# Performance work log

Hardware: AMD Instinct MI355X
Metric: run time of the kernel (lower is better)

Reference implementation:

```python
import jax, jax.numpy as jnp
import numpy as np

N_NODES = 100000
N_EDGES = 1000000
D = 64  # gat_input_size == gat_hidden_size
NEG_SLOPE = 0.2  # PyG GATConv default leaky_relu slope


def setup_inputs() -> dict:
    key = jax.random.key(0)
    k1, k2, k3, k4, k5, k6 = jax.random.split(key, 6)
    g = jax.random.normal(k1, (N_NODES, D), dtype=jnp.float32)
    edge_index = jax.random.randint(k2, (2, N_EDGES), 0, N_NODES, dtype=jnp.int32)
    scale = 1.0 / np.sqrt(D)
    W = jax.random.normal(k3, (D, D), dtype=jnp.float32) * scale
    att_src = jax.random.normal(k4, (D,), dtype=jnp.float32) * scale
    att_dst = jax.random.normal(k5, (D,), dtype=jnp.float32) * scale
    bias = jnp.zeros((D,), dtype=jnp.float32)
    return {"g": g, "edge_index": edge_index, "W": W,
            "att_src": att_src, "att_dst": att_dst, "bias": bias}


def _gat_layer(x, src, dst, W, att_src, att_dst, bias):
    N = x.shape[0]
    h = x @ W                               # [N, D] projected features
    a_src = h @ att_src                     # [N] per-node source logits
    a_dst = h @ att_dst                     # [N] per-node target logits
    e = jax.nn.leaky_relu(a_src[src] + a_dst[dst], NEG_SLOPE)  # [E]
    # numerically stable segment softmax over edges grouped by target node
    m = jax.ops.segment_max(e, dst, num_segments=N)            # [N]
    m = jnp.where(jnp.isfinite(m), m, 0.0)                     # isolated nodes
    ex = jnp.exp(e - m[dst])                                   # [E]
    denom = jax.ops.segment_sum(ex, dst, num_segments=N)       # [N]
    alpha = ex / (denom[dst] + 1e-16)                          # [E]
    out = jax.ops.segment_sum(alpha[:, None] * h[src], dst, num_segments=N)
    return out + bias


def reference(g, edge_index, W, att_src, att_dst, bias):
    src, dst = edge_index[0], edge_index[1]
    for _ in range(4):  # same shared GAT applied 4 times
        g = _gat_layer(g, src, dst, W, att_src, att_dst, bias)
    return g
```

## Files before the change

### kernel.cpp

```cpp
#include <hip/hip_runtime.h>
#include <hip/hip_bf16.h>

typedef unsigned int u32;
typedef unsigned short u16;
typedef unsigned long long u64;
typedef __attribute__((ext_vector_type(8))) short short8;
typedef __attribute__((ext_vector_type(4))) float f32x4;
typedef __attribute__((ext_vector_type(2))) float f32x2;

#define LRELU_SLOPE 0.2f
#define BPB 32
#define MAXPER 13000

__device__ inline float bfbits(u32 hi) { union { u32 i; float f; } v; v.i = hi; return v.f; }
__device__ inline float bflo(u32 w) { return bfbits(w << 16); }
__device__ inline float bfhi(u32 w) { return bfbits(w & 0xFFFF0000u); }
__device__ inline float bf2f(u16 s) { return bfbits(((u32)s) << 16); }
__device__ inline u16 f2bf(float f) {
  union { float f; u32 i; } v; v.f = f;
  u32 r = v.i + 0x7FFFu + ((v.i >> 16) & 1u);
  return (u16)(r >> 16);
}
__device__ inline f32x2 up2(u32 w) { return (f32x2){bflo(w), bfhi(w)}; }

__device__ inline int xcd_swz(int orig, int nwg) {
  int xcd = orig & 7, idx = orig >> 3;
  int q = nwg >> 3, r = nwg & 7;
  return (xcd < r ? xcd * (q + 1) : r * (q + 1) + (xcd - r) * q) + idx;
}

__global__ void dp_kernel(const u32* __restrict__ g, int nwords, int* __restrict__ mode,
                          const void* __restrict__ W, const void* __restrict__ as,
                          const void* __restrict__ ad, const void* __restrict__ bs,
                          float* __restrict__ pf, u16* __restrict__ wfrag,
                          int* __restrict__ gcnt) {
  __shared__ int cnt;
  if (threadIdx.x == 0) cnt = 0;
  if (threadIdx.x < 8) gcnt[threadIdx.x] = 0;
  __syncthreads();
  int c = 0;
  for (int i = threadIdx.x; i < nwords; i += 256) {
    u32 e = g[i] & 0x7F80u;
    if (e >= 0x3000u && e <= 0x4180u) c++;
  }
  atomicAdd(&cnt, c);
  __syncthreads();
  int md = (2 * cnt > nwords) ? 1 : 0;
  if (threadIdx.x == 0) *mode = md;

  for (int i = threadIdx.x; i < 4288; i += 256) {
    const void* p; int j;
    if (i < 4096)      { p = W;  j = i; }
    else if (i < 4160) { p = as; j = i - 4096; }
    else if (i < 4224) { p = ad; j = i - 4160; }
    else               { p = bs; j = i - 4224; }
    pf[i] = md ? bf2f(((const u16*)p)[j]) : ((const float*)p)[j];
  }
  __syncthreads();
  for (int i = threadIdx.x; i < 4096; i += 256) {
    int f = i >> 9, lane = (i >> 3) & 63, j = i & 7;
    int cc = f >> 1, t = f & 1;
    int k = 32 * t + 8 * (lane >> 4) + j;
    int n = 16 * cc + (lane & 15);
    wfrag[i] = f2bf(pf[k * 64 + n]);
  }
}

__device__ void binA_body(const int* __restrict__ src, const int* __restrict__ dst,
                          int* __restrict__ gcnt, uint2* __restrict__ binned,
                          int E, int nper, int cap, int bid) {
  __shared__ int lcnt[8], lbase[8], lcur[8];
  const int K = 8;
  int tile0 = bid * (256 * K);
  int t = threadIdx.x;
  if (t < 8) { lcnt[t] = 0; lcur[t] = 0; }
  __syncthreads();
  int dv[K], sv[K], bv[K];
#pragma unroll
  for (int j = 0; j < K; ++j) {
    int idx = tile0 + j * 256 + t;
    bool ok = idx < E;
    int d = ok ? __builtin_nontemporal_load(&dst[idx]) : 0;
    int s = ok ? __builtin_nontemporal_load(&src[idx]) : 0;
    int b = -1;
    if (ok) {
      b = (d >= 4 * nper) ? 4 : 0;
      if (d >= (b + 2) * nper) b += 2;
      if (d >= (b + 1) * nper) b += 1;
      atomicAdd(&lcnt[b], 1);
    }
    dv[j] = d; sv[j] = s; bv[j] = b;
  }
  __syncthreads();
  if (t < 8) lbase[t] = atomicAdd(&gcnt[t], lcnt[t]);
  __syncthreads();
#pragma unroll
  for (int j = 0; j < K; ++j) {
    int b = bv[j];
    if (b >= 0) {
      int slot = lbase[b] + atomicAdd(&lcur[b], 1);
      if (slot < cap) binned[(size_t)b * cap + slot] = make_uint2((u32)sv[j], (u32)dv[j]);
    }
  }
}

__device__ void proj0_body(const void* __restrict__ graw, const int* __restrict__ mode,
                           const u16* __restrict__ wfrag, const float* __restrict__ pf,
                           u16* __restrict__ h0, u16* __restrict__ h1,
                           float* __restrict__ as0, float* __restrict__ as1,
                           float* __restrict__ ad0, int N, int bid, int pblocks) {
  if (bid == 0) {
    if (threadIdx.x < 32)       ((u32*)(h0 + (size_t)N * 64))[threadIdx.x] = 0u;
    else if (threadIdx.x < 64)  ((u32*)(h1 + (size_t)N * 64))[threadIdx.x - 32] = 0u;
    else if (threadIdx.x == 64) as0[N] = -1e30f;
    else if (threadIdx.x == 65) as1[N] = -1e30f;
  }
  int lane = threadIdx.x & 63;
  int quad = lane >> 4, m = lane & 15;
  int wtile = (int)(((size_t)bid * 256 + threadIdx.x) >> 6);
  int ntiles = (N + 15) >> 4;
  int nwaves = pblocks * 4;

  int md = *mode;
  bool f32in = (md == 0);

  short8 bfrag[8];
#pragma unroll
  for (int f = 0; f < 8; ++f)
    bfrag[f] = *(const short8*)(wfrag + f * 512 + lane * 8);
  float asv[4], adv[4];
#pragma unroll
  for (int c = 0; c < 4; ++c) {
    asv[c] = pf[4096 + 16 * c + m];
    adv[c] = pf[4160 + 16 * c + m];
  }

  for (int tile = wtile; tile < ntiles; tile += nwaves) {
    int row0 = tile << 4;
    int rl = row0 + m; if (rl > N - 1) rl = N - 1;
    short8 a0, a1;
    if (f32in) {
      const float* xr = (const float*)graw + (size_t)rl * 64 + 8 * quad;
      float4 f0 = *(const float4*)(xr);
      float4 f1 = *(const float4*)(xr + 4);
      float4 f2 = *(const float4*)(xr + 32);
      float4 f3 = *(const float4*)(xr + 36);
      a0[0] = (short)f2bf(f0.x); a0[1] = (short)f2bf(f0.y);
      a0[2] = (short)f2bf(f0.z); a0[3] = (short)f2bf(f0.w);
      a0[4] = (short)f2bf(f1.x); a0[5] = (short)f2bf(f1.y);
      a0[6] = (short)f2bf(f1.z); a0[7] = (short)f2bf(f1.w);
      a1[0] = (short)f2bf(f2.x); a1[1] = (short)f2bf(f2.y);
      a1[2] = (short)f2bf(f2.z); a1[3] = (short)f2bf(f2.w);
      a1[4] = (short)f2bf(f3.x); a1[5] = (short)f2bf(f3.y);
      a1[6] = (short)f2bf(f3.z); a1[7] = (short)f2bf(f3.w);
    } else {
      const u16* xr = (const u16*)graw + (size_t)rl * 64 + 8 * quad;
      a0 = *(const short8*)(xr);
      a1 = *(const short8*)(xr + 32);
    }

    f32x4 acc[4];
#pragma unroll
    for (int c = 0; c < 4; ++c) {
      f32x4 z = {0.f, 0.f, 0.f, 0.f};
      z = __builtin_amdgcn_mfma_f32_16x16x32_bf16(a0, bfrag[2 * c + 0], z, 0, 0, 0);
      z = __builtin_amdgcn_mfma_f32_16x16x32_bf16(a1, bfrag[2 * c + 1], z, 0, 0, 0);
      acc[c] = z;
    }

#pragma unroll
    for (int r = 0; r < 4; ++r) {
      int row = row0 + 4 * quad + r;
      float v0 = acc[0][r], v1 = acc[1][r], v2 = acc[2][r], v3 = acc[3][r];
      if (row < N) {
        u16* hr = h0 + (size_t)row * 64 + m;
        hr[0]  = f2bf(v0);
        hr[16] = f2bf(v1);
        hr[32] = f2bf(v2);
        hr[48] = f2bf(v3);
      }
      float s1 = v0 * asv[0] + v1 * asv[1] + v2 * asv[2] + v3 * asv[3];
      float s2 = v0 * adv[0] + v1 * adv[1] + v2 * adv[2] + v3 * adv[3];
#pragma unroll
      for (int msk = 1; msk <= 8; msk <<= 1) {
        s1 += __shfl_xor(s1, msk, 64);
        s2 += __shfl_xor(s2, msk, 64);
      }
      if (m == 0 && row < N) { as0[row] = s1; ad0[row] = s2; }
    }
  }
}

__global__ void __launch_bounds__(256) fatBP_kernel(
    const int* __restrict__ src, const int* __restrict__ dst, int* __restrict__ gcnt,
    uint2* __restrict__ binned, int E, int nper, int cap, int abl,
    const void* __restrict__ graw, const int* __restrict__ mode,
    const u16* __restrict__ wfrag, const float* __restrict__ pf,
    u16* __restrict__ h0, u16* __restrict__ h1,
    float* __restrict__ as0, float* __restrict__ as1,
    float* __restrict__ ad0, int N) {
  if ((int)blockIdx.x < abl) {
    binA_body(src, dst, gcnt, binned, E, nper, cap, (int)blockIdx.x);
  } else {
    proj0_body(graw, mode, wfrag, pf, h0, h1, as0, as1, ad0, N,
               (int)blockIdx.x - abl, (int)gridDim.x - abl);
  }
}

__global__ void __launch_bounds__(256) binA_kernel(
    const int* __restrict__ src, const int* __restrict__ dst, int* __restrict__ gcnt,
    uint2* __restrict__ binned, int E, int nper, int cap) {
  binA_body(src, dst, gcnt, binned, E, nper, cap, (int)blockIdx.x);
}
__global__ void __launch_bounds__(256) proj0_kernel(
    const void* __restrict__ graw, const int* __restrict__ mode,
    const u16* __restrict__ wfrag, const float* __restrict__ pf,
    u16* __restrict__ h0, u16* __restrict__ h1,
    float* __restrict__ as0, float* __restrict__ as1,
    float* __restrict__ ad0, int N) {
  proj0_body(graw, mode, wfrag, pf, h0, h1, as0, as1, ad0, N,
             (int)blockIdx.x, (int)gridDim.x);
}

__global__ void __launch_bounds__(256) histA_kernel(
    const uint2* __restrict__ binned, const int* __restrict__ gcnt,
    u32* __restrict__ slices, int nper, int cap) {
  __shared__ u32 cnt_lds[MAXPER];
  int b = blockIdx.x & 7;
  int j = blockIdx.x >> 3;
  int cnt = gcnt[b]; if (cnt > cap) cnt = cap;
  int chunk = (cnt + BPB - 1) / BPB;
  int begin = j * chunk;
  int endc = begin + chunk; if (endc > cnt) endc = cnt;
  for (int k = threadIdx.x; k < nper; k += 256) cnt_lds[k] = 0;
  __syncthreads();
  const uint2* reg = binned + (size_t)b * cap;
  int kbase = b * nper;
  for (int i = begin + threadIdx.x; i < endc; i += 256)
    atomicAdd(&cnt_lds[(int)reg[i].y - kbase], 1u);
  __syncthreads();
  u32* out = slices + (size_t)(b * BPB + j) * nper;
  for (int k = threadIdx.x; k < nper; k += 256) out[k] = cnt_lds[k];
}

__global__ void scan1f_kernel(const u32* __restrict__ slices, int* __restrict__ row_off,
                              int* __restrict__ partials, int nper, int N) {
  __shared__ int smem[1024];
  int t = threadIdx.x;
  int idx = blockIdx.x * 1024 + t;
  int v = 0;
  if (idx < N) {
    int b = idx / nper;
    int kk = idx - b * nper;
    const u32* s = slices + (size_t)b * BPB * nper + kk;
    u32 tt = 0;
#pragma unroll 8
    for (int j = 0; j < BPB; ++j) tt += s[(size_t)j * nper];
    v = (int)((tt + 7u) & ~7u);
  }
  smem[t] = v;
  __syncthreads();
  for (int off = 1; off < 1024; off <<= 1) {
    int u = (t >= off) ? smem[t - off] : 0;
    __syncthreads();
    smem[t] += u;
    __syncthreads();
  }
  if (idx < N) row_off[idx + 1] = smem[t];
  if (t == 1023) partials[blockIdx.x] = smem[t];
}

__global__ void scan3c_kernel(int* __restrict__ row_off, const int* __restrict__ partials,
                              int P, u32* __restrict__ slices, int* __restrict__ csr_src,
                              int nper, int N, int dummy) {
  __shared__ int smem[1024];
  int t = threadIdx.x;
  int pv = (t < P) ? partials[t] : 0;
  smem[t] = pv;
  __syncthreads();
  for (int off = 1; off < 1024; off <<= 1) {
    int u = (t >= off) ? smem[t - off] : 0;
    __syncthreads();
    smem[t] += u;
    __syncthreads();
  }
  int blk = blockIdx.x;
  int prefix = (blk > 0) ? smem[blk - 1] : 0;
  int idx = blk * 1024 + t;
  if (idx == 0) row_off[0] = 0;
  if (idx < N) {
    int vend = row_off[idx + 1] + prefix;
    row_off[idx + 1] = vend;
    int b = idx / nper;
    int kk = idx - b * nper;
    u32* s = slices + (size_t)b * BPB * nper + kk;
    u32 tv[BPB];
    u32 deg = 0;
#pragma unroll
    for (int j = 0; j < BPB; ++j) { tv[j] = s[(size_t)j * nper]; deg += tv[j]; }
    u32 pdeg = (deg + 7u) & ~7u;
    u32 run = (u32)vend - pdeg;
#pragma unroll
    for (int j = 0; j < BPB; ++j) { s[(size_t)j * nper] = run; run += tv[j]; }
    for (u32 p = run; p < (u32)vend; ++p) csr_src[p] = dummy;
  }
}

__global__ void __launch_bounds__(256) scatterB_kernel(
    const uint2* __restrict__ binned, const int* __restrict__ gcnt,
    const u32* __restrict__ slices, int* __restrict__ csr_src, int nper, int cap) {
  __shared__ u32 base_lds[MAXPER];
  int b = blockIdx.x & 7;
  int j = blockIdx.x >> 3;
  int cnt = gcnt[b]; if (cnt > cap) cnt = cap;
  int chunk = (cnt + BPB - 1) / BPB;
  int begin = j * chunk;
  int endc = begin + chunk; if (endc > cnt) endc = cnt;
  const u32* s = slices + (size_t)(b * BPB + j) * nper;
  for (int k = threadIdx.x; k < nper; k += 256) base_lds[k] = s[k];
  __syncthreads();
  const uint2* reg = binned + (size_t)b * cap;
  int kbase = b * nper;
  for (int i = begin + threadIdx.x; i < endc; i += 256) {
    uint2 r = reg[i];
    u32 p = atomicAdd(&base_lds[(int)r.y - kbase], 1u);
    csr_src[p] = (int)r.x;
  }
}

__global__ void hist_local_kernel(const uint2* __restrict__ binned, const int* __restrict__ gcnt,
                                  int* __restrict__ deg, int cap) {
  int b = blockIdx.x & 7;
  int vb = blockIdx.x >> 3, nvb = gridDim.x >> 3;
  int cnt = gcnt[b]; if (cnt > cap) cnt = cap;
  const uint2* reg = binned + (size_t)b * cap;
  for (int i = vb * blockDim.x + threadIdx.x; i < cnt; i += nvb * blockDim.x)
    atomicAdd(&deg[reg[i].y], 1);
}

__global__ void scatter_local_kernel(const uint2* __restrict__ binned, const int* __restrict__ gcnt,
                                     int* __restrict__ cursor, int* __restrict__ csr_src, int cap) {
  int b = blockIdx.x & 7;
  int vb = blockIdx.x >> 3, nvb = gridDim.x >> 3;
  int cnt = gcnt[b]; if (cnt > cap) cnt = cap;
  const uint2* reg = binned + (size_t)b * cap;
  for (int i = vb * blockDim.x + threadIdx.x; i < cnt; i += nvb * blockDim.x) {
    uint2 r = reg[i];
    int p = atomicAdd(&cursor[r.y], 1);
    csr_src[p] = (int)r.x;
  }
}

__global__ void scan1_kernel(const int* __restrict__ deg, int* __restrict__ row_off,
                             int* __restrict__ partials, int N) {
  __shared__ int smem[1024];
  int t = threadIdx.x;
  int idx = blockIdx.x * 1024 + t;
  int v = (idx < N) ? (int)(((u32)deg[idx] + 7u) & ~7u) : 0;
  smem[t] = v;
  __syncthreads();
  for (int off = 1; off < 1024; off <<= 1) {
    int u = (t >= off) ? smem[t - off] : 0;
    __syncthreads();
    smem[t] += u;
    __syncthreads();
  }
  if (idx < N) row_off[idx + 1] = smem[t];
  if (t == 1023) partials[blockIdx.x] = smem[t];
}

__global__ void scan2_kernel(int* __restrict__ partials, int P) {
  __shared__ int smem[1024];
  int t = threadIdx.x;
  int v = (t < P) ? partials[t] : 0;
  smem[t] = v;
  __syncthreads();
  for (int off = 1; off < 1024; off <<= 1) {
    int u = (t >= off) ? smem[t - off] : 0;
    __syncthreads();
    smem[t] += u;
    __syncthreads();
  }
  if (t < P) partials[t] = smem[t];
}

__global__ void scan3_kernel(int* __restrict__ row_off, const int* __restrict__ partials,
                             int* __restrict__ cursor, int N) {
  int b = blockIdx.x;
  int idx = b * 1024 + threadIdx.x;
  if (idx < N) {
    int v = row_off[idx + 1] + ((b > 0) ? partials[b - 1] : 0);
    row_off[idx + 1] = v;
    if (idx + 1 < N) cursor[idx + 1] = v;
  }
  if (idx == 0) { row_off[0] = 0; cursor[0] = 0; }
}

__global__ void padC_kernel(const int* __restrict__ row_off, const int* __restrict__ cursor,
                            int* __restrict__ csr_src, int N, int dummy) {
  int i = blockIdx.x * blockDim.x + threadIdx.x;
  if (i >= N) return;
  int e = row_off[i + 1];
  for (int p = cursor[i]; p < e; ++p) csr_src[p] = dummy;
}

__global__ void __launch_bounds__(256) fusedFG_kernel(
    const u16* __restrict__ hin, const float* __restrict__ asi,
    const float* __restrict__ adi, u16* __restrict__ hout,
    float* __restrict__ aso, float* __restrict__ ado,
    const int* __restrict__ row_off, const int* __restrict__ csr_src,
    const float* __restrict__ pf, const u16* __restrict__ wfrag, int N) {
  __shared__ u16 xs[16][72];
  __shared__ float sred[2][16][4];

  int tid = threadIdx.x;
  int lane = tid & 63;
  int w = tid >> 6;
  int quad = lane >> 4, m = lane & 15;
  int grp = lane >> 4;
  int eg = (lane >> 3) & 1;
  int fg = lane & 7;
  int tile = xcd_swz((int)blockIdx.x, (int)gridDim.x);
  int row_in = w * 4 + grp;
  int i = tile * 16 + row_in;
  bool valid = i < N;

  short8 bf0 = *(const short8*)(wfrag + (2 * w + 0) * 512 + lane * 8);
  short8 bf1 = *(const short8*)(wfrag + (2 * w + 1) * 512 + lane * 8);
  float asw = pf[4096 + 16 * w + m];
  float adw = pf[4160 + 16 * w + m];

  int beg = 0, end = 0;
  float advv = 0.f;
  if (valid) { beg = row_off[i]; end = row_off[i + 1]; advv = adi[i]; }

  f32x2 acc0 = {0.f, 0.f}, acc1 = {0.f, 0.f}, acc2 = {0.f, 0.f}, acc3 = {0.f, 0.f};
  float den = 0.f;
  for (int b0 = beg; b0 < end; b0 += 8) {
    int eA = b0 + eg;
    int sA = csr_src[eA];
    int sB = csr_src[eA + 2];
    int sC = csr_src[eA + 4];
    int sD = csr_src[eA + 6];
    float aA = asi[sA];
    float aB = asi[sB];
    float aC = asi[sC];
    float aD = asi[sD];
    uint4 hA = ((const uint4*)(hin + (size_t)sA * 64))[fg];
    uint4 hB = ((const uint4*)(hin + (size_t)sB * 64))[fg];
    uint4 hC = ((const uint4*)(hin + (size_t)sC * 64))[fg];
    uint4 hD = ((const uint4*)(hin + (size_t)sD * 64))[fg];

    float tA = aA + advv; tA = (tA > 0.f) ? tA : LRELU_SLOPE * tA;
    float tB = aB + advv; tB = (tB > 0.f) ? tB : LRELU_SLOPE * tB;
    float tC = aC + advv; tC = (tC > 0.f) ? tC : LRELU_SLOPE * tC;
    float tD = aD + advv; tD = (tD > 0.f) ? tD : LRELU_SLOPE * tD;
    float wA = __expf(fminf(tA, 60.f));
    float wB = __expf(fminf(tB, 60.f));
    float wC = __expf(fminf(tC, 60.f));
    float wD = __expf(fminf(tD, 60.f));
    den += (wA + wB) + (wC + wD);
    f32x2 wA2 = {wA, wA}, wB2 = {wB, wB}, wC2 = {wC, wC}, wD2 = {wD, wD};
    acc0 += wA2 * up2(hA.x); acc0 += wB2 * up2(hB.x);
    acc0 += wC2 * up2(hC.x); acc0 += wD2 * up2(hD.x);
    acc1 += wA2 * up2(hA.y); acc1 += wB2 * up2(hB.y);
    acc1 += wC2 * up2(hC.y); acc1 += wD2 * up2(hD.y);
    acc2 += wA2 * up2(hA.z); acc2 += wB2 * up2(hB.z);
    acc2 += wC2 * up2(hC.z); acc2 += wD2 * up2(hD.z);
    acc3 += wA2 * up2(hA.w); acc3 += wB2 * up2(hB.w);
    acc3 += wC2 * up2(hC.w); acc3 += wD2 * up2(hD.w);
  }
  den += __shfl_xor(den, 8, 64);
#pragma unroll
  for (int c = 0; c < 2; ++c) {
    acc0[c] += __shfl_xor(acc0[c], 8, 64);
    acc1[c] += __shfl_xor(acc1[c], 8, 64);
    acc2[c] += __shfl_xor(acc2[c], 8, 64);
    acc3[c] += __shfl_xor(acc3[c], 8, 64);
  }
  float inv = (den > 0.f) ? 1.f / den : 0.f;
  float oa[8] = {acc0[0], acc0[1], acc1[0], acc1[1],
                 acc2[0], acc2[1], acc3[0], acc3[1]};

  if (!eg) {
    u32 o[4];
    if (valid) {
#pragma unroll
      for (int j = 0; j < 4; ++j) {
        float v0 = oa[2 * j]     * inv + pf[4224 + 8 * fg + 2 * j];
        float v1 = oa[2 * j + 1] * inv + pf[4224 + 8 * fg + 2 * j + 1];
        o[j] = (u32)f2bf(v0) | ((u32)f2bf(v1) << 16);
      }
    } else {
      o[0] = o[1] = o[2] = o[3] = 0u;
    }
    *(uint4*)&xs[row_in][fg * 8] = make_uint4(o[0], o[1], o[2], o[3]);
  }
  __syncthreads();

  short8 a0 = *(const short8*)&xs[m][8 * quad];
  short8 a1 = *(const short8*)&xs[m][32 + 8 * quad];
  f32x4 z = {0.f, 0.f, 0.f, 0.f};
  z = __builtin_amdgcn_mfma_f32_16x16x32_bf16(a0, bf0, z, 0, 0, 0);
  z = __builtin_amdgcn_mfma_f32_16x16x32_bf16(a1, bf1, z, 0, 0, 0);
#pragma unroll
  for (int r = 0; r < 4; ++r) {
    int row = tile * 16 + 4 * quad + r;
    if (row < N) hout[(size_t)row * 64 + 16 * w + m] = f2bf(z[r]);
    float s1 = z[r] * asw, s2 = z[r] * adw;
#pragma unroll
    for (int msk = 1; msk <= 8; msk <<= 1) {
      s1 += __shfl_xor(s1, msk, 64);
      s2 += __shfl_xor(s2, msk, 64);
    }
    if (m == 0) { sred[0][4 * quad + r][w] = s1; sred[1][4 * quad + r][w] = s2; }
  }
  __syncthreads();
  if (tid < 32) {
    int row = tid & 15, sel = tid >> 4;
    float v = sred[sel][row][0] + sred[sel][row][1] + sred[sel][row][2] + sred[sel][row][3];
    int gr = tile * 16 + row;
    if (gr < N) (sel ? ado : aso)[gr] = v;
  }
}

__global__ void __launch_bounds__(256) gatherL_kernel(
    const u16* __restrict__ h, const float* __restrict__ a_src,
    const float* __restrict__ a_dst, const int* __restrict__ row_off,
    const int* __restrict__ csr_src, const float* __restrict__ pf,
    void* __restrict__ dout, int N, const int* __restrict__ mode) {
  int lane = threadIdx.x & 63;
  int grp = lane >> 4;
  int eg  = (lane >> 3) & 1;
  int fg  = lane & 7;
  int w   = threadIdx.x >> 6;
  int tile = xcd_swz((int)blockIdx.x, (int)gridDim.x);
  int i = tile * 16 + w * 4 + grp;
  bool valid = i < N;

  int beg = 0, end = 0;
  float adv = 0.f;
  if (valid) {
    beg = row_off[i];
    end = row_off[i + 1];
    adv = a_dst[i];
  }

  f32x2 acc0 = {0.f, 0.f}, acc1 = {0.f, 0.f}, acc2 = {0.f, 0.f}, acc3 = {0.f, 0.f};
  float den = 0.f;

  for (int b0 = beg; b0 < end; b0 += 8) {
    int eA = b0 + eg;
    int sA = csr_src[eA];
    int sB = csr_src[eA + 2];
    int sC = csr_src[eA + 4];
    int sD = csr_src[eA + 6];
    float aA = a_src[sA];
    float aB = a_src[sB];
    float aC = a_src[sC];
    float aD = a_src[sD];
    uint4 hA = ((const uint4*)(h + (size_t)sA * 64))[fg];
    uint4 hB = ((const uint4*)(h + (size_t)sB * 64))[fg];
    uint4 hC = ((const uint4*)(h + (size_t)sC * 64))[fg];
    uint4 hD = ((const uint4*)(h + (size_t)sD * 64))[fg];

    float tA = aA + adv; tA = (tA > 0.f) ? tA : LRELU_SLOPE * tA;
    float tB = aB + adv; tB = (tB > 0.f) ? tB : LRELU_SLOPE * tB;
    float tC = aC + adv; tC = (tC > 0.f) ? tC : LRELU_SLOPE * tC;
    float tD = aD + adv; tD = (tD > 0.f) ? tD : LRELU_SLOPE * tD;
    float wA = __expf(fminf(tA, 60.f));
    float wB = __expf(fminf(tB, 60.f));
    float wC = __expf(fminf(tC, 60.f));
    float wD = __expf(fminf(tD, 60.f));
    den += (wA + wB) + (wC + wD);
    f32x2 wA2 = {wA, wA}, wB2 = {wB, wB}, wC2 = {wC, wC}, wD2 = {wD, wD};
    acc0 += wA2 * up2(hA.x); acc0 += wB2 * up2(hB.x);
    acc0 += wC2 * up2(hC.x); acc0 += wD2 * up2(hD.x);
    acc1 += wA2 * up2(hA.y); acc1 += wB2 * up2(hB.y);
    acc1 += wC2 * up2(hC.y); acc1 += wD2 * up2(hD.y);
    acc2 += wA2 * up2(hA.z); acc2 += wB2 * up2(hB.z);
    acc2 += wC2 * up2(hC.z); acc2 += wD2 * up2(hD.z);
    acc3 += wA2 * up2(hA.w); acc3 += wB2 * up2(hB.w);
    acc3 += wC2 * up2(hC.w); acc3 += wD2 * up2(hD.w);
  }

  den += __shfl_xor(den, 8, 64);
#pragma unroll
  for (int c = 0; c < 2; ++c) {
    acc0[c] += __shfl_xor(acc0[c], 8, 64);
    acc1[c] += __shfl_xor(acc1[c], 8, 64);
    acc2[c] += __shfl_xor(acc2[c], 8, 64);
    acc3[c] += __shfl_xor(acc3[c], 8, 64);
  }
  float inv = (den > 0.f) ? 1.f / den : 0.f;

  if (!valid || eg) return;

  float oa[8] = {acc0[0], acc0[1], acc1[0], acc1[1], acc2[0], acc2[1], acc3[0], acc3[1]};
  if (*mode) {
    u32 o[4];
#pragma unroll
    for (int j = 0; j < 4; ++j) {
      float f0 = oa[2 * j]     * inv + pf[4224 + 8 * fg + 2 * j];
      float f1 = oa[2 * j + 1] * inv + pf[4224 + 8 * fg + 2 * j + 1];
      o[j] = (u32)f2bf(f0) | ((u32)f2bf(f1) << 16);
    }
    *(uint4*)((u16*)dout + (size_t)i * 64 + fg * 8) = make_uint4(o[0], o[1], o[2], o[3]);
  } else {
    float o[8];
#pragma unroll
    for (int j = 0; j < 8; ++j)
      o[j] = oa[j] * inv + pf[4224 + 8 * fg + j];
    float* dp = (float*)dout + (size_t)i * 64 + fg * 8;
    *(float4*)(dp)     = make_float4(o[0], o[1], o[2], o[3]);
    *(float4*)(dp + 4) = make_float4(o[4], o[5], o[6], o[7]);
  }
}

extern "C" void kernel_launch(void* const* d_in, const int* in_sizes, int n_in,
                              void* d_out, int out_size, void* d_ws, size_t ws_size,
                              hipStream_t stream) {
  const void* g     = d_in[0];
  const int*  edge  = (const int*)d_in[1];
  const void* Wp    = d_in[2];
  const void* attsp = d_in[3];
  const void* attdp = d_in[4];
  const void* biasp = d_in[5];

  const int D = 64;
  const int N = in_sizes[0] / D;
  const int E = in_sizes[1] / 2;
  const int* src = edge;
  const int* dst = edge + E;

  int nper = (N + 7) / 8;
  bool fast_csr = (nper <= MAXPER);

  char* ws = (char*)d_ws;
  size_t off = 0;
  auto alloc = [&](size_t bytes) -> char* {
    char* p = ws + off;
    off += (bytes + 255) & ~size_t(255);
    return p;
  };
  size_t h_bytes = (size_t)(N + 1) * D * sizeof(u16);
  u16*   h0       = (u16*)alloc(h_bytes);
  u16*   h1       = (u16*)alloc(h_bytes);
  u32*   slices   = (u32*)alloc((size_t)8 * BPB * nper * sizeof(u32));
  float* pf       = (float*)alloc(4288 * sizeof(float));
  u16*   wfrag    = (u16*)alloc(4096 * sizeof(u16));
  float* as0      = (float*)alloc((size_t)(N + 1) * sizeof(float));
  float* as1      = (float*)alloc((size_t)(N + 1) * sizeof(float));
  float* ad0      = (float*)alloc((size_t)N * sizeof(float));
  float* ad1      = (float*)alloc((size_t)N * sizeof(float));
  int*   deg      = (int*)alloc((size_t)N * sizeof(int));
  int*   row_off  = (int*)alloc((size_t)(N + 1) * sizeof(int));
  int*   cursor   = (int*)alloc((size_t)N * sizeof(int));
  int*   csr_src  = (int*)alloc(((size_t)E + 8 * (size_t)N) * sizeof(int));
  int*   partials = (int*)alloc(1024 * sizeof(int));
  int*   mode     = (int*)alloc(256);
  int*   gcnt     = (int*)alloc(256);
  int    cap      = E / 8 + 16384;
  uint2* binned   = (uint2*)alloc((size_t)8 * cap * sizeof(uint2));

  dp_kernel<<<1, 256, 0, stream>>>((const u32*)g, 4096, mode, Wp, attsp, attdp, biasp,
                                   pf, wfrag, gcnt);

  if (!fast_csr) hipMemsetAsync(deg, 0, (size_t)N * sizeof(int), stream);
  int abl = (E + 2047) / 2048;
  int ntiles = (N + 15) / 16;
  int tblocks = (ntiles + 3) / 4;

  int nblk = (N + 1023) / 1024;
  if (fast_csr) {
    fatBP_kernel<<<abl + tblocks, 256, 0, stream>>>(
        src, dst, gcnt, binned, E, nper, cap, abl,
        g, mode, wfrag, pf, h0, h1, as0, as1, ad0, N);
    histA_kernel<<<8 * BPB, 256, 0, stream>>>(binned, gcnt, slices, nper, cap);
    scan1f_kernel<<<nblk, 1024, 0, stream>>>(slices, row_off, partials, nper, N);
    scan3c_kernel<<<nblk, 1024, 0, stream>>>(row_off, partials, nblk, slices, csr_src,
                                             nper, N, N);
    scatterB_kernel<<<8 * BPB, 256, 0, stream>>>(binned, gcnt, slices, csr_src, nper, cap);
  } else {
    binA_kernel<<<abl, 256, 0, stream>>>(src, dst, gcnt, binned, E, nper, cap);
    hist_local_kernel<<<1024, 256, 0, stream>>>(binned, gcnt, deg, cap);
    scan1_kernel<<<nblk, 1024, 0, stream>>>(deg, row_off, partials, N);
    scan2_kernel<<<1, 1024, 0, stream>>>(partials, nblk);
    scan3_kernel<<<nblk, 1024, 0, stream>>>(row_off, partials, cursor, N);
    scatter_local_kernel<<<1024, 256, 0, stream>>>(binned, gcnt, cursor, csr_src, cap);
    padC_kernel<<<(N + 255) / 256, 256, 0, stream>>>(row_off, cursor, csr_src, N, N);
    proj0_kernel<<<tblocks, 256, 0, stream>>>(g, mode, wfrag, pf, h0, h1, as0, as1, ad0, N);
  }

  fusedFG_kernel<<<ntiles, 256, 0, stream>>>(h0, as0, ad0, h1, as1, ad1,
                                             row_off, csr_src, pf, wfrag, N);
  fusedFG_kernel<<<ntiles, 256, 0, stream>>>(h1, as1, ad1, h0, as0, ad0,
                                             row_off, csr_src, pf, wfrag, N);
  fusedFG_kernel<<<ntiles, 256, 0, stream>>>(h0, as0, ad0, h1, as1, ad1,
                                             row_off, csr_src, pf, wfrag, N);

  gatherL_kernel<<<ntiles, 256, 0, stream>>>(h1, as1, ad1, row_off, csr_src, pf,
                                             d_out, N, mode);
}
```

Baseline: 261.2 us.

## Prestage per-edge attention weights and source indices in LDS before gather

Both gather kernels gain a prologue in which 16 threads per destination row read the CSR source indices and compute the leaky-ReLU/exp edge weights for up to 64 edges. The results are stored as (weight, src) pairs in shared memory, followed by a block barrier. The main loop then reads these pairs from LDS and issues only the feature-row loads, so it no longer repeats the exp on every feature lane or waits on the csr→a_src dependent load chain per edge. Rows with more than 64 edges fall back to the original loop for the remainder. The cost is an extra LDS buffer and a __syncthreads, and the prologue keeps its own serial dependent loads.

```diff
diff --git a/kernel.cpp b/kernel.cpp
--- a/kernel.cpp
+++ b/kernel.cpp
@@ -11,6 +11,7 @@
 #define LRELU_SLOPE 0.2f
 #define BPB 32
 #define MAXPER 13000
+#define WSTAGE 64
 
 __device__ inline float bfbits(u32 hi) { union { u32 i; float f; } v; v.i = hi; return v.f; }
 __device__ inline float bflo(u32 w) { return bfbits(w << 16); }
@@ -412,6 +413,7 @@
     const float* __restrict__ pf, const u16* __restrict__ wfrag, int N) {
   __shared__ u16 xs[16][72];
   __shared__ float sred[2][16][4];
+  __shared__ uint2 lwP[16][WSTAGE + 1];
 
   int tid = threadIdx.x;
   int lane = tid & 63;
@@ -430,13 +432,62 @@
   float asw = pf[4096 + 16 * w + m];
   float adw = pf[4160 + 16 * w + m];
 
+  {
+    int pr = tid >> 4, pl = tid & 15;
+    int ir = tile * 16 + pr;
+    if (ir < N) {
+      int rb = row_off[ir];
+      int lim = row_off[ir + 1] - rb;
+      if (lim > WSTAGE) lim = WSTAGE;
+      float adv_r = adi[ir];
+      for (int j = pl; j < lim; j += 16) {
+        int s = csr_src[rb + j];
+        float a = asi[s];
+        float t = a + adv_r;
+        t = (t > 0.f) ? t : LRELU_SLOPE * t;
+        float wv = __expf(fminf(t, 60.f));
+        lwP[pr][j] = make_uint2(__float_as_uint(wv), (u32)s);
+      }
+    }
+  }
+  __syncthreads();
+
   int beg = 0, end = 0;
   float advv = 0.f;
   if (valid) { beg = row_off[i]; end = row_off[i + 1]; advv = adi[i]; }
 
   f32x2 acc0 = {0.f, 0.f}, acc1 = {0.f, 0.f}, acc2 = {0.f, 0.f}, acc3 = {0.f, 0.f};
   float den = 0.f;
-  for (int b0 = beg; b0 < end; b0 += 8) {
+
+  int pd = end - beg;
+  int lim = pd < WSTAGE ? pd : WSTAGE;
+  for (int o = 0; o < lim; o += 8) {
+    int j = o + eg;
+    uint2 pA = lwP[row_in][j];
+    uint2 pB = lwP[row_in][j + 2];
+    uint2 pC = lwP[row_in][j + 4];
+    uint2 pD = lwP[row_in][j + 6];
+    float wA = __uint_as_float(pA.x); int sA = (int)pA.y;
+    float wB = __uint_as_float(pB.x); int sB = (int)pB.y;
+    float wC = __uint_as_float(pC.x); int sC = (int)pC.y;
+    float wD = __uint_as_float(pD.x); int sD = (int)pD.y;
+    uint4 hA = ((const uint4*)(hin + (size_t)sA * 64))[fg];
+    uint4 hB = ((const uint4*)(hin + (size_t)sB * 64))[fg];
+    uint4 hC = ((const uint4*)(hin + (size_t)sC * 64))[fg];
+    uint4 hD = ((const uint4*)(hin + (size_t)sD * 64))[fg];
+
+    den += (wA + wB) + (wC + wD);
+    f32x2 wA2 = {wA, wA}, wB2 = {wB, wB}, wC2 = {wC, wC}, wD2 = {wD, wD};
+    acc0 += wA2 * up2(hA.x); acc0 += wB2 * up2(hB.x);
+    acc0 += wC2 * up2(hC.x); acc0 += wD2 * up2(hD.x);
+    acc1 += wA2 * up2(hA.y); acc1 += wB2 * up2(hB.y);
+    acc1 += wC2 * up2(hC.y); acc1 += wD2 * up2(hD.y);
+    acc2 += wA2 * up2(hA.z); acc2 += wB2 * up2(hB.z);
+    acc2 += wC2 * up2(hC.z); acc2 += wD2 * up2(hD.z);
+    acc3 += wA2 * up2(hA.w); acc3 += wB2 * up2(hB.w);
+    acc3 += wC2 * up2(hC.w); acc3 += wD2 * up2(hD.w);
+  }
+  for (int b0 = beg + WSTAGE; b0 < end; b0 += 8) {
     int eA = b0 + eg;
     int sA = csr_src[eA];
     int sB = csr_src[eA + 2];
@@ -450,7 +501,6 @@
     uint4 hB = ((const uint4*)(hin + (size_t)sB * 64))[fg];
     uint4 hC = ((const uint4*)(hin + (size_t)sC * 64))[fg];
     uint4 hD = ((const uint4*)(hin + (size_t)sD * 64))[fg];
-
     float tA = aA + advv; tA = (tA > 0.f) ? tA : LRELU_SLOPE * tA;
     float tB = aB + advv; tB = (tB > 0.f) ? tB : LRELU_SLOPE * tB;
     float tC = aC + advv; tC = (tC > 0.f) ? tC : LRELU_SLOPE * tC;
@@ -470,6 +520,7 @@
     acc3 += wA2 * up2(hA.w); acc3 += wB2 * up2(hB.w);
     acc3 += wC2 * up2(hC.w); acc3 += wD2 * up2(hD.w);
   }
+
   den += __shfl_xor(den, 8, 64);
 #pragma unroll
   for (int c = 0; c < 2; ++c) {
@@ -529,14 +580,37 @@
     const float* __restrict__ a_dst, const int* __restrict__ row_off,
     const int* __restrict__ csr_src, const float* __restrict__ pf,
     void* __restrict__ dout, int N, const int* __restrict__ mode) {
-  int lane = threadIdx.x & 63;
+  __shared__ uint2 lwP[16][WSTAGE + 1];
+  int tid = threadIdx.x;
+  int lane = tid & 63;
   int grp = lane >> 4;
   int eg  = (lane >> 3) & 1;
   int fg  = lane & 7;
-  int w   = threadIdx.x >> 6;
+  int w   = tid >> 6;
   int tile = xcd_swz((int)blockIdx.x, (int)gridDim.x);
-  int i = tile * 16 + w * 4 + grp;
+  int row_in = w * 4 + grp;
+  int i = tile * 16 + row_in;
   bool valid = i < N;
+
+  {
+    int pr = tid >> 4, pl = tid & 15;
+    int ir = tile * 16 + pr;
+    if (ir < N) {
+      int rb = row_off[ir];
+      int lim = row_off[ir + 1] - rb;
+      if (lim > WSTAGE) lim = WSTAGE;
+      float adv_r = a_dst[ir];
+      for (int j = pl; j < lim; j += 16) {
+        int s = csr_src[rb + j];
+        float a = a_src[s];
+        float t = a + adv_r;
+        t = (t > 0.f) ? t : LRELU_SLOPE * t;
+        float wv = __expf(fminf(t, 60.f));
+        lwP[pr][j] = make_uint2(__float_as_uint(wv), (u32)s);
+      }
+    }
+  }
+  __syncthreads();
 
   int beg = 0, end = 0;
   float adv = 0.f;
@@ -549,7 +623,35 @@
   f32x2 acc0 = {0.f, 0.f}, acc1 = {0.f, 0.f}, acc2 = {0.f, 0.f}, acc3 = {0.f, 0.f};
   float den = 0.f;
 
-  for (int b0 = beg; b0 < end; b0 += 8) {
+  int pd = end - beg;
+  int lim = pd < WSTAGE ? pd : WSTAGE;
+  for (int o = 0; o < lim; o += 8) {
+    int j = o + eg;
+    uint2 pA = lwP[row_in][j];
+    uint2 pB = lwP[row_in][j + 2];
+    uint2 pC = lwP[row_in][j + 4];
+    uint2 pD = lwP[row_in][j + 6];
+    float wA = __uint_as_float(pA.x); int sA = (int)pA.y;
+    float wB = __uint_as_float(pB.x); int sB = (int)pB.y;
+    float wC = __uint_as_float(pC.x); int sC = (int)pC.y;
+    float wD = __uint_as_float(pD.x); int sD = (int)pD.y;
+    uint4 hA = ((const uint4*)(h + (size_t)sA * 64))[fg];
+    uint4 hB = ((const uint4*)(h + (size_t)sB * 64))[fg];
+    uint4 hC = ((const uint4*)(h + (size_t)sC * 64))[fg];
+    uint4 hD = ((const uint4*)(h + (size_t)sD * 64))[fg];
+
+    den += (wA + wB) + (wC + wD);
+    f32x2 wA2 = {wA, wA}, wB2 = {wB, wB}, wC2 = {wC, wC}, wD2 = {wD, wD};
+    acc0 += wA2 * up2(hA.x); acc0 += wB2 * up2(hB.x);
+    acc0 += wC2 * up2(hC.x); acc0 += wD2 * up2(hD.x);
+    acc1 += wA2 * up2(hA.y); acc1 += wB2 * up2(hB.y);
+    acc1 += wC2 * up2(hC.y); acc1 += wD2 * up2(hD.y);
+    acc2 += wA2 * up2(hA.z); acc2 += wB2 * up2(hB.z);
+    acc2 += wC2 * up2(hC.z); acc2 += wD2 * up2(hD.z);
+    acc3 += wA2 * up2(hA.w); acc3 += wB2 * up2(hB.w);
+    acc3 += wC2 * up2(hC.w); acc3 += wD2 * up2(hD.w);
+  }
+  for (int b0 = beg + WSTAGE; b0 < end; b0 += 8) {
     int eA = b0 + eg;
     int sA = csr_src[eA];
     int sB = csr_src[eA + 2];
@@ -563,7 +665,6 @@
     uint4 hB = ((const uint4*)(h + (size_t)sB * 64))[fg];
     uint4 hC = ((const uint4*)(h + (size_t)sC * 64))[fg];
     uint4 hD = ((const uint4*)(h + (size_t)sD * 64))[fg];
-
     float tA = aA + adv; tA = (tA > 0.f) ? tA : LRELU_SLOPE * tA;
     float tB = aB + adv; tB = (tB > 0.f) ? tB : LRELU_SLOPE * tB;
     float tC = aC + adv; tC = (tC > 0.f) ? tC : LRELU_SLOPE * tC;
```

Measured after the change: 269.4 us. +3.2%, slower.
